# Performance work log

Hardware: AMD Instinct MI355X
Metric: run time of the kernel (lower is better)

The kernel has to match this reference:

```python
import jax, jax.numpy as jnp
import numpy as np

IN_CH_IMG = 256
CHANNELS = 256
NUM_CLASSES = 1
NUM_LAYERS = 4  # NUM_FC=3 -> 4 layers
IN_CH = IN_CH_IMG + 256  # pos-enc adds 256 channels
N_INST = 128
N_PTS = 2048

W_SIZES = [IN_CH * CHANNELS, CHANNELS * CHANNELS, CHANNELS * CHANNELS, CHANNELS * NUM_CLASSES]
B_SIZES = [CHANNELS, CHANNELS, CHANNELS, NUM_CLASSES]
NUM_PARAMS = sum(W_SIZES) + sum(B_SIZES)  # 263169


def setup_inputs() -> dict:
    key = jax.random.key(0)
    k1, k2, k3, k4 = jax.random.split(key, 4)
    return {
        "fine_grained_features": jax.random.normal(k1, (N_INST, IN_CH_IMG, N_PTS), dtype=jnp.float32),
        "point_coords": jax.random.uniform(k2, (N_INST, N_PTS, 2), dtype=jnp.float32),
        "parameters": jax.random.normal(k3, (N_INST, NUM_PARAMS), dtype=jnp.float32) * 0.05,
        "pe_gaussian": jax.random.normal(k4, (2, 128), dtype=jnp.float32),
    }


def _parse_params(params):
    # params: [N, NUM_PARAMS]. Weight blocks first, then bias blocks.
    n = params.shape[0]
    out_dims = [CHANNELS, CHANNELS, CHANNELS, NUM_CLASSES]
    in_dims = [IN_CH, CHANNELS, CHANNELS, CHANNELS]
    weights, biases = [], []
    off = 0
    for l in range(NUM_LAYERS):
        weights.append(params[:, off:off + W_SIZES[l]].reshape(n, out_dims[l], in_dims[l]))
        off += W_SIZES[l]
    for l in range(NUM_LAYERS):
        biases.append(params[:, off:off + B_SIZES[l]].reshape(n, out_dims[l], 1))
        off += B_SIZES[l]
    return weights, biases


def reference(fine_grained_features, point_coords, parameters, pe_gaussian):
    n, _, p = fine_grained_features.shape
    # Positional encoding: [N*P, 2] -> [N*P, 128] -> sin/cos -> [N, 256, P]
    loc = (2.0 * point_coords.reshape(n * p, 2) - 1.0) @ pe_gaussian
    loc = 2.0 * np.pi * loc
    pe = jnp.concatenate([jnp.sin(loc), jnp.cos(loc)], axis=1)  # [N*P, 256]
    pe = pe.reshape(n, p, 256).transpose(0, 2, 1)  # [N, 256, P]
    x = jnp.concatenate([pe, fine_grained_features], axis=1)  # [N, IN_CH, P]

    weights, biases = _parse_params(parameters)
    for i, (w, b) in enumerate(zip(weights, biases)):
        x = jnp.einsum('nck,ndc->ndk', x, w) + b
        if i < NUM_LAYERS - 1:
            x = jax.nn.relu(x)
    return x.reshape(-1, NUM_CLASSES, p)  # [N, 1, P]
```

## Files before the change

### kernel.cpp

```cpp
#include <hip/hip_runtime.h>
#include <hip/hip_fp16.h>


#define NI      128
#define NPTS    2048
#define CH      256
#define NPARAM  263169
#define PT      64
#define NTILES  (NPTS / PT)
#define ROWS    536

#define WOFF0   0
#define WOFF1   131072
#define WOFF2   196608
#define WOFF3   262144
#define BOFF0   262400
#define BOFF1   262656
#define BOFF2   262912
#define BOFF3   263168

#define PI_L0   0
#define PI_L1   131072
#define PI_L2   196608
#define PI_L3   262144
#define WS_PER_INST 262400
#define WS_BYTES ((size_t)NI * WS_PER_INST * 2)

typedef __fp16   h16x2 __attribute__((ext_vector_type(2)));
typedef _Float16 f16x8 __attribute__((ext_vector_type(8)));
typedef float    f32x4 __attribute__((ext_vector_type(4)));

union pack8 { h16x2 h[4]; f16x8 v; };

__global__ __launch_bounds__(256) void iph_prep(
    const float* __restrict__ params, _Float16* __restrict__ wsw)
{
    const int inst = blockIdx.y;
    const int r = blockIdx.x * 256 + threadIdx.x;
    if (r >= 32800) return;
    const float* __restrict__ P = params + (size_t)inst * NPARAM;
    _Float16* __restrict__ W = wsw + (size_t)inst * WS_PER_INST;

    int rl, woff, K, dst;
    if (r < 16384)      { rl = r;         woff = WOFF0; K = 512; dst = PI_L0; }
    else if (r < 24576) { rl = r - 16384; woff = WOFF1; K = 256; dst = PI_L1; }
    else if (r < 32768) { rl = r - 24576; woff = WOFF2; K = 256; dst = PI_L2; }
    else {
        const int e = (r - 32768) * 8;
        f16x8 v;
        #pragma unroll
        for (int j = 0; j < 8; ++j) v[j] = (_Float16)P[WOFF3 + e + j];
        *(f16x8*)&W[PI_L3 + e] = v;
        return;
    }
    const int e    = rl * 8;
    const int lane = rl & 63;
    const int cb   = (rl >> 6) & 15;
    const int ks   = rl >> 10;
    const int co   = (cb >> 1) * 32 + 2 * (lane & 15) + (cb & 1);
    const int k    = ks * 32 + (lane >> 4) * 8;
    const float* __restrict__ src = P + woff + co * K + k;
    f16x8 v;
    #pragma unroll
    for (int j = 0; j < 8; ++j) v[j] = (_Float16)src[j];
    *(f16x8*)&W[dst + e] = v;
}

__device__ __forceinline__ void issue_b2(const _Float16* p, f16x8& r0, f16x8& r1) {
    const unsigned long long a = (unsigned long long)p;
    asm volatile("global_load_dwordx4 %0, %2, off\n\t"
                 "global_load_dwordx4 %1, %2, off offset:1024"
                 : "=&v"(r0), "=&v"(r1)
                 : "v"(a));
}

template<int N>
__device__ __forceinline__ void wait_vm() {
    if constexpr (N >= 8)      asm volatile("s_waitcnt vmcnt(8)" ::: "memory");
    else if constexpr (N == 6) asm volatile("s_waitcnt vmcnt(6)" ::: "memory");
    else if constexpr (N == 4) asm volatile("s_waitcnt vmcnt(4)" ::: "memory");
    else if constexpr (N == 2) asm volatile("s_waitcnt vmcnt(2)" ::: "memory");
    else                       asm volatile("s_waitcnt vmcnt(0)" ::: "memory");
    __builtin_amdgcn_sched_barrier(0);
}

__device__ __forceinline__ void lgkm0_barrier() {
    asm volatile("s_waitcnt lgkmcnt(0)" ::: "memory");
    __builtin_amdgcn_s_barrier();
}

__device__ __forceinline__ void issue_pro(const _Float16* bp, f16x8 (&b0s)[5], f16x8 (&b1s)[5]) {
    #pragma unroll
    for (int i = 0; i < 4; ++i)
        issue_b2(bp + i * 8192, b0s[i], b1s[i]);
}

template<int NKS>
__device__ __forceinline__ void gemm_pipe(
    f32x4 (&acc)[4][2], const _Float16* bp, const _Float16* ap,
    f16x8 (&b0s)[5], f16x8 (&b1s)[5])
{
    #pragma unroll
    for (int ks = 0; ks < NKS; ++ks) {
        f16x8 a0 = *(const f16x8*)(ap + ks * 32);
        f16x8 a1 = *(const f16x8*)(ap + 16 * ROWS + ks * 32);
        f16x8 a2 = *(const f16x8*)(ap + 32 * ROWS + ks * 32);
        f16x8 a3 = *(const f16x8*)(ap + 48 * ROWS + ks * 32);
        if (ks + 4 < NKS)
            issue_b2(bp + (ks + 4) * 8192, b0s[(ks + 4) % 5], b1s[(ks + 4) % 5]);
        const int rem = NKS - 1 - ks;
        if (rem >= 4)      wait_vm<8>();
        else if (rem == 3) wait_vm<6>();
        else if (rem == 2) wait_vm<4>();
        else if (rem == 1) wait_vm<2>();
        else               wait_vm<0>();
        __builtin_amdgcn_s_setprio(1);
        acc[0][0] = __builtin_amdgcn_mfma_f32_16x16x32_f16(a0, b0s[ks % 5], acc[0][0], 0, 0, 0);
        acc[0][1] = __builtin_amdgcn_mfma_f32_16x16x32_f16(a0, b1s[ks % 5], acc[0][1], 0, 0, 0);
        acc[1][0] = __builtin_amdgcn_mfma_f32_16x16x32_f16(a1, b0s[ks % 5], acc[1][0], 0, 0, 0);
        acc[1][1] = __builtin_amdgcn_mfma_f32_16x16x32_f16(a1, b1s[ks % 5], acc[1][1], 0, 0, 0);
        acc[2][0] = __builtin_amdgcn_mfma_f32_16x16x32_f16(a2, b0s[ks % 5], acc[2][0], 0, 0, 0);
        acc[2][1] = __builtin_amdgcn_mfma_f32_16x16x32_f16(a2, b1s[ks % 5], acc[2][1], 0, 0, 0);
        acc[3][0] = __builtin_amdgcn_mfma_f32_16x16x32_f16(a3, b0s[ks % 5], acc[3][0], 0, 0, 0);
        acc[3][1] = __builtin_amdgcn_mfma_f32_16x16x32_f16(a3, b1s[ks % 5], acc[3][1], 0, 0, 0);
        __builtin_amdgcn_s_setprio(0);
    }
}

template<bool PREPPED>
__global__ __launch_bounds__(512, 4) void iph_main(
    const float* __restrict__ feat,
    const float* __restrict__ coords,
    const float* __restrict__ params,
    const _Float16* __restrict__ wsw,
    const float* __restrict__ peg,
    float* __restrict__ out)
{
    __shared__ _Float16 X[PT * ROWS];
    __shared__ float    partial[8][PT];

    const int bid  = blockIdx.x;
    const int inst = (bid & 7) | ((bid >> 8) << 3);
    const int tile = (bid >> 3) & 31;
    const int p0   = tile * PT;
    const int tid  = threadIdx.x;
    const int lane = tid & 63;
    const int wave = tid >> 6;
    const int l15  = lane & 15;
    const int hi   = lane >> 4;
    const float* __restrict__ P = params + (size_t)inst * NPARAM;
    const _Float16* __restrict__ WI = wsw + (size_t)inst * WS_PER_INST;

    const _Float16* bp0 = WI + PI_L0 + ((wave * 2) * 64 + lane) * 8;
    const _Float16* bp1 = WI + PI_L1 + ((wave * 2) * 64 + lane) * 8;
    const _Float16* bp2 = WI + PI_L2 + ((wave * 2) * 64 + lane) * 8;
    const _Float16* ap  = &X[l15 * ROWS + hi * 8];

    f16x8 s0[5], s1[5], t0[5], t1[5], u0[5], u1[5];

    if (PREPPED) issue_pro(bp0, s0, s1);

    {
        const int pt   = tid >> 3;
        const int part = tid & 7;
        const float2 cc = *(const float2*)&coords[((size_t)inst * NPTS + p0 + pt) * 2];
        const float a = 2.f * cc.x - 1.f;
        const float b = 2.f * cc.y - 1.f;
        float sv[16], cv[16];
        #pragma unroll
        for (int j = 0; j < 16; ++j) {
            const int f = part * 16 + j;
            float locr = a * peg[f] + b * peg[128 + f];
            locr -= floorf(locr);
            sv[j] = __builtin_amdgcn_sinf(locr);
            cv[j] = __builtin_amdgcn_cosf(locr);
        }
        pack8 q0, q1, c0, c1;
        #pragma unroll
        for (int q = 0; q < 4; ++q) {
            q0.h[q] = __builtin_amdgcn_cvt_pkrtz(sv[2*q],     sv[2*q + 1]);
            q1.h[q] = __builtin_amdgcn_cvt_pkrtz(sv[8 + 2*q], sv[9 + 2*q]);
            c0.h[q] = __builtin_amdgcn_cvt_pkrtz(cv[2*q],     cv[2*q + 1]);
            c1.h[q] = __builtin_amdgcn_cvt_pkrtz(cv[8 + 2*q], cv[9 + 2*q]);
        }
        _Float16* base = &X[pt * ROWS + part * 16];
        *(f16x8*)(base)           = q0.v;
        *(f16x8*)(base + 8)       = q1.v;
        *(f16x8*)(base + 128)     = c0.v;
        *(f16x8*)(base + 136)     = c1.v;
    }
    {
        const float* fbase = feat + (size_t)inst * CH * NPTS + p0 + lane;
        #pragma unroll
        for (int s = 0; s < 4; ++s) {
            const int c0i = s * 64 + wave * 8;
            float w8[8];
            #pragma unroll
            for (int j = 0; j < 8; ++j)
                w8[j] = fbase[(size_t)(c0i + j) * NPTS];
            pack8 pk;
            #pragma unroll
            for (int q = 0; q < 4; ++q)
                pk.h[q] = __builtin_amdgcn_cvt_pkrtz(w8[2*q], w8[2*q + 1]);
            *(f16x8*)&X[lane * ROWS + 256 + c0i] = pk.v;
        }
    }
    lgkm0_barrier();

    auto write_epilogue = [&](f32x4 (&acc)[4][2], const float2 bb) {
        #pragma unroll
        for (int mt = 0; mt < 4; ++mt) {
            #pragma unroll
            for (int r = 0; r < 4; ++r) {
                const float v0 = fmaxf(acc[mt][0][r] + bb.x, 0.f);
                const float v1 = fmaxf(acc[mt][1][r] + bb.y, 0.f);
                const h16x2 e = __builtin_amdgcn_cvt_pkrtz(v0, v1);
                const int pt = mt * 16 + hi * 4 + r;
                *(h16x2*)&X[pt * ROWS + wave * 32 + 2 * l15] = e;
            }
        }
    };

    auto gemm_simple = [&](f32x4 (&acc)[4][2], const float* pw, const int K) {
        for (int ks = 0; ks < (K >> 5); ++ks) {
            f16x8 bfrag[2];
            #pragma unroll
            for (int nt = 0; nt < 2; ++nt) {
                const int co = wave * 32 + 2 * l15 + nt;
                const float* wp = pw + (size_t)co * K + ks * 32 + hi * 8;
                float w8[8];
                __builtin_memcpy(w8, wp, 32);
                f16x8 bb;
                #pragma unroll
                for (int j = 0; j < 8; ++j) bb[j] = (_Float16)w8[j];
                bfrag[nt] = bb;
            }
            f16x8 afrag[4];
            #pragma unroll
            for (int mt = 0; mt < 4; ++mt)
                afrag[mt] = *(const f16x8*)&X[(mt * 16 + l15) * ROWS + ks * 32 + hi * 8];
            #pragma unroll
            for (int mt = 0; mt < 4; ++mt)
                #pragma unroll
                for (int nt = 0; nt < 2; ++nt)
                    acc[mt][nt] = __builtin_amdgcn_mfma_f32_16x16x32_f16(
                        afrag[mt], bfrag[nt], acc[mt][nt], 0, 0, 0);
        }
    };

    {
        f32x4 acc[4][2];
        #pragma unroll
        for (int mt = 0; mt < 4; ++mt)
            #pragma unroll
            for (int nt = 0; nt < 2; ++nt)
                acc[mt][nt] = (f32x4){0.f, 0.f, 0.f, 0.f};
        const float2 bb = *(const float2*)&P[BOFF0 + wave * 32 + 2 * l15];
        if (PREPPED) gemm_pipe<16>(acc, bp0, ap, s0, s1);
        else         gemm_simple(acc, P + WOFF0, 512);
        if (PREPPED) issue_pro(bp1, t0, t1);
        __builtin_amdgcn_s_barrier();
        write_epilogue(acc, bb);
        lgkm0_barrier();
    }
    {
        f32x4 acc[4][2];
        #pragma unroll
        for (int mt = 0; mt < 4; ++mt)
            #pragma unroll
            for (int nt = 0; nt < 2; ++nt)
                acc[mt][nt] = (f32x4){0.f, 0.f, 0.f, 0.f};
        const float2 bb = *(const float2*)&P[BOFF1 + wave * 32 + 2 * l15];
        if (PREPPED) gemm_pipe<8>(acc, bp1, ap, t0, t1);
        else         gemm_simple(acc, P + WOFF1, 256);
        if (PREPPED) issue_pro(bp2, u0, u1);
        __builtin_amdgcn_s_barrier();
        write_epilogue(acc, bb);
        lgkm0_barrier();
    }
    {
        f32x4 acc[4][2];
        #pragma unroll
        for (int mt = 0; mt < 4; ++mt)
            #pragma unroll
            for (int nt = 0; nt < 2; ++nt)
                acc[mt][nt] = (f32x4){0.f, 0.f, 0.f, 0.f};
        const float2 bb = *(const float2*)&P[BOFF2 + wave * 32 + 2 * l15];
        const float2 w3 = *(const float2*)&P[WOFF3 + wave * 32 + 2 * l15];
        if (PREPPED) gemm_pipe<8>(acc, bp2, ap, u0, u1);
        else         gemm_simple(acc, P + WOFF2, 256);
        #pragma unroll
        for (int mt = 0; mt < 4; ++mt) {
            #pragma unroll
            for (int r = 0; r < 4; ++r) {
                const float v0 = fmaxf(acc[mt][0][r] + bb.x, 0.f);
                const float v1 = fmaxf(acc[mt][1][r] + bb.y, 0.f);
                float s = v0 * w3.x + v1 * w3.y;
                s += __shfl_xor(s, 1);
                s += __shfl_xor(s, 2);
                s += __shfl_xor(s, 4);
                s += __shfl_xor(s, 8);
                if (l15 == 0)
                    partial[wave][mt * 16 + hi * 4 + r] = s;
            }
        }
        lgkm0_barrier();
        if (tid < PT) {
            float s = P[BOFF3];
            #pragma unroll
            for (int w = 0; w < 8; ++w) s += partial[w][tid];
            out[(size_t)inst * NPTS + p0 + tid] = s;
        }
    }
}

extern "C" void kernel_launch(void* const* d_in, const int* in_sizes, int n_in,
                              void* d_out, int out_size, void* d_ws, size_t ws_size,
                              hipStream_t stream) {
    (void)in_sizes; (void)n_in; (void)out_size;
    const float* feat   = (const float*)d_in[0];
    const float* coords = (const float*)d_in[1];
    const float* params = (const float*)d_in[2];
    const float* peg    = (const float*)d_in[3];
    float* out = (float*)d_out;

    dim3 grid(NI * NTILES);
    dim3 block(512);

    if (ws_size >= WS_BYTES) {
        _Float16* wsw = (_Float16*)d_ws;
        iph_prep<<<dim3(129, 128), dim3(256), 0, stream>>>(params, wsw);
        iph_main<true><<<grid, block, 0, stream>>>(feat, coords, params, wsw, peg, out);
    } else {
        iph_main<false><<<grid, block, 0, stream>>>(feat, coords, params,
                                                    (const _Float16*)d_ws, peg, out);
    }
}
```

Before: 214.9 us.

## Switch GEMM layers to 32x32x16 MFMA with 8-deep single-load weight pipeline

Replaces the 16x16x32 MFMA tiling (4x2 accumulator tiles per wave) with two 32x32x16 MFMAs per k-step. The prepacked weight layout, LDS A-fragment addressing, epilogue and final reduction are reworked to match. The weight prefetch becomes one dwordx4 load per k-step with an 8-deep ring instead of paired loads 4 deep, and bias loads are hoisted to the kernel start. The aim is fewer MFMA issues and LDS A-reads per FLOP. In exchange the epilogue now writes scalar fp16 values to LDS instead of packed pairs, and k-steps are smaller.

After: 264.6 us. 1.23x slower.

```diff
diff --git a/kernel.cpp b/kernel.cpp
--- a/kernel.cpp
+++ b/kernel.cpp
@@ -26,9 +26,9 @@
 #define WS_PER_INST 262400
 #define WS_BYTES ((size_t)NI * WS_PER_INST * 2)
 
-typedef __fp16   h16x2 __attribute__((ext_vector_type(2)));
-typedef _Float16 f16x8 __attribute__((ext_vector_type(8)));
-typedef float    f32x4 __attribute__((ext_vector_type(4)));
+typedef __fp16   h16x2  __attribute__((ext_vector_type(2)));
+typedef _Float16 f16x8  __attribute__((ext_vector_type(8)));
+typedef float    f32x16 __attribute__((ext_vector_type(16)));
 
 union pack8 { h16x2 h[4]; f16x8 v; };
 
@@ -55,10 +55,10 @@
     }
     const int e    = rl * 8;
     const int lane = rl & 63;
-    const int cb   = (rl >> 6) & 15;
-    const int ks   = rl >> 10;
-    const int co   = (cb >> 1) * 32 + 2 * (lane & 15) + (cb & 1);
-    const int k    = ks * 32 + (lane >> 4) * 8;
+    const int cb   = (rl >> 6) & 7;
+    const int ks   = rl >> 9;
+    const int co   = cb * 32 + (lane & 31);
+    const int k    = ks * 16 + (lane >> 5) * 8;
     const float* __restrict__ src = P + woff + co * K + k;
     f16x8 v;
     #pragma unroll
@@ -66,20 +66,20 @@
     *(f16x8*)&W[dst + e] = v;
 }
 
-__device__ __forceinline__ void issue_b2(const _Float16* p, f16x8& r0, f16x8& r1) {
+__device__ __forceinline__ void issue_b1(const _Float16* p, f16x8& r0) {
     const unsigned long long a = (unsigned long long)p;
-    asm volatile("global_load_dwordx4 %0, %2, off\n\t"
-                 "global_load_dwordx4 %1, %2, off offset:1024"
-                 : "=&v"(r0), "=&v"(r1)
-                 : "v"(a));
+    asm volatile("global_load_dwordx4 %0, %1, off" : "=&v"(r0) : "v"(a));
 }
 
 template<int N>
 __device__ __forceinline__ void wait_vm() {
-    if constexpr (N >= 8)      asm volatile("s_waitcnt vmcnt(8)" ::: "memory");
+    if constexpr (N >= 7)      asm volatile("s_waitcnt vmcnt(7)" ::: "memory");
     else if constexpr (N == 6) asm volatile("s_waitcnt vmcnt(6)" ::: "memory");
+    else if constexpr (N == 5) asm volatile("s_waitcnt vmcnt(5)" ::: "memory");
     else if constexpr (N == 4) asm volatile("s_waitcnt vmcnt(4)" ::: "memory");
+    else if constexpr (N == 3) asm volatile("s_waitcnt vmcnt(3)" ::: "memory");
     else if constexpr (N == 2) asm volatile("s_waitcnt vmcnt(2)" ::: "memory");
+    else if constexpr (N == 1) asm volatile("s_waitcnt vmcnt(1)" ::: "memory");
     else                       asm volatile("s_waitcnt vmcnt(0)" ::: "memory");
     __builtin_amdgcn_sched_barrier(0);
 }
@@ -89,41 +89,35 @@
     __builtin_amdgcn_s_barrier();
 }
 
-__device__ __forceinline__ void issue_pro(const _Float16* bp, f16x8 (&b0s)[5], f16x8 (&b1s)[5]) {
+__device__ __forceinline__ void issue_pro8(const _Float16* bp, f16x8 (&q)[8]) {
     #pragma unroll
-    for (int i = 0; i < 4; ++i)
-        issue_b2(bp + i * 8192, b0s[i], b1s[i]);
+    for (int i = 0; i < 8; ++i) issue_b1(bp + i * 4096, q[i]);
 }
 
 template<int NKS>
 __device__ __forceinline__ void gemm_pipe(
-    f32x4 (&acc)[4][2], const _Float16* bp, const _Float16* ap,
-    f16x8 (&b0s)[5], f16x8 (&b1s)[5])
+    f32x16& acc0, f32x16& acc1, const _Float16* bp, const _Float16* ap,
+    f16x8 (&q)[8])
 {
     #pragma unroll
     for (int ks = 0; ks < NKS; ++ks) {
-        f16x8 a0 = *(const f16x8*)(ap + ks * 32);
-        f16x8 a1 = *(const f16x8*)(ap + 16 * ROWS + ks * 32);
-        f16x8 a2 = *(const f16x8*)(ap + 32 * ROWS + ks * 32);
-        f16x8 a3 = *(const f16x8*)(ap + 48 * ROWS + ks * 32);
-        if (ks + 4 < NKS)
-            issue_b2(bp + (ks + 4) * 8192, b0s[(ks + 4) % 5], b1s[(ks + 4) % 5]);
+        f16x8 a0 = *(const f16x8*)(ap + ks * 16);
+        f16x8 a1 = *(const f16x8*)(ap + 32 * ROWS + ks * 16);
         const int rem = NKS - 1 - ks;
-        if (rem >= 4)      wait_vm<8>();
-        else if (rem == 3) wait_vm<6>();
-        else if (rem == 2) wait_vm<4>();
-        else if (rem == 1) wait_vm<2>();
+        if (rem >= 7)      wait_vm<7>();
+        else if (rem == 6) wait_vm<6>();
+        else if (rem == 5) wait_vm<5>();
+        else if (rem == 4) wait_vm<4>();
+        else if (rem == 3) wait_vm<3>();
+        else if (rem == 2) wait_vm<2>();
+        else if (rem == 1) wait_vm<1>();
         else               wait_vm<0>();
         __builtin_amdgcn_s_setprio(1);
-        acc[0][0] = __builtin_amdgcn_mfma_f32_16x16x32_f16(a0, b0s[ks % 5], acc[0][0], 0, 0, 0);
-        acc[0][1] = __builtin_amdgcn_mfma_f32_16x16x32_f16(a0, b1s[ks % 5], acc[0][1], 0, 0, 0);
-        acc[1][0] = __builtin_amdgcn_mfma_f32_16x16x32_f16(a1, b0s[ks % 5], acc[1][0], 0, 0, 0);
-        acc[1][1] = __builtin_amdgcn_mfma_f32_16x16x32_f16(a1, b1s[ks % 5], acc[1][1], 0, 0, 0);
-        acc[2][0] = __builtin_amdgcn_mfma_f32_16x16x32_f16(a2, b0s[ks % 5], acc[2][0], 0, 0, 0);
-        acc[2][1] = __builtin_amdgcn_mfma_f32_16x16x32_f16(a2, b1s[ks % 5], acc[2][1], 0, 0, 0);
-        acc[3][0] = __builtin_amdgcn_mfma_f32_16x16x32_f16(a3, b0s[ks % 5], acc[3][0], 0, 0, 0);
-        acc[3][1] = __builtin_amdgcn_mfma_f32_16x16x32_f16(a3, b1s[ks % 5], acc[3][1], 0, 0, 0);
+        acc0 = __builtin_amdgcn_mfma_f32_32x32x16_f16(a0, q[ks & 7], acc0, 0, 0, 0);
+        acc1 = __builtin_amdgcn_mfma_f32_32x32x16_f16(a1, q[ks & 7], acc1, 0, 0, 0);
         __builtin_amdgcn_s_setprio(0);
+        if (ks + 8 < NKS)
+            issue_b1(bp + (ks + 8) * 4096, q[ks & 7]);
     }
 }
 
@@ -146,19 +140,24 @@
     const int tid  = threadIdx.x;
     const int lane = tid & 63;
     const int wave = tid >> 6;
-    const int l15  = lane & 15;
-    const int hi   = lane >> 4;
+    const int l31  = lane & 31;
+    const int sel  = lane >> 5;
     const float* __restrict__ P = params + (size_t)inst * NPARAM;
     const _Float16* __restrict__ WI = wsw + (size_t)inst * WS_PER_INST;
 
-    const _Float16* bp0 = WI + PI_L0 + ((wave * 2) * 64 + lane) * 8;
-    const _Float16* bp1 = WI + PI_L1 + ((wave * 2) * 64 + lane) * 8;
-    const _Float16* bp2 = WI + PI_L2 + ((wave * 2) * 64 + lane) * 8;
-    const _Float16* ap  = &X[l15 * ROWS + hi * 8];
-
-    f16x8 s0[5], s1[5], t0[5], t1[5], u0[5], u1[5];
-
-    if (PREPPED) issue_pro(bp0, s0, s1);
+    const _Float16* bp0 = WI + PI_L0 + (wave * 64 + lane) * 8;
+    const _Float16* bp1 = WI + PI_L1 + (wave * 64 + lane) * 8;
+    const _Float16* bp2 = WI + PI_L2 + (wave * 64 + lane) * 8;
+    const _Float16* ap  = &X[l31 * ROWS + sel * 8];
+
+    const float bb0 = P[BOFF0 + wave * 32 + l31];
+    const float bb1 = P[BOFF1 + wave * 32 + l31];
+    const float bb2 = P[BOFF2 + wave * 32 + l31];
+    const float w3  = P[WOFF3 + wave * 32 + l31];
+
+    f16x8 qa[8], qb[8], qc[8];
+
+    if (PREPPED) issue_pro8(bp0, qa);
 
     {
         const int pt   = tid >> 3;
@@ -207,101 +206,69 @@
     }
     lgkm0_barrier();
 
-    auto write_epilogue = [&](f32x4 (&acc)[4][2], const float2 bb) {
-        #pragma unroll
-        for (int mt = 0; mt < 4; ++mt) {
-            #pragma unroll
-            for (int r = 0; r < 4; ++r) {
-                const float v0 = fmaxf(acc[mt][0][r] + bb.x, 0.f);
-                const float v1 = fmaxf(acc[mt][1][r] + bb.y, 0.f);
-                const h16x2 e = __builtin_amdgcn_cvt_pkrtz(v0, v1);
-                const int pt = mt * 16 + hi * 4 + r;
-                *(h16x2*)&X[pt * ROWS + wave * 32 + 2 * l15] = e;
+    auto write_epilogue = [&](const f32x16& a0, const f32x16& a1, const float bb) {
+        #pragma unroll
+        for (int r = 0; r < 16; ++r) {
+            const int ptrow = (r & 3) + 8 * (r >> 2) + 4 * sel;
+            const float v0 = fmaxf(a0[r] + bb, 0.f);
+            const float v1 = fmaxf(a1[r] + bb, 0.f);
+            X[ptrow * ROWS + wave * 32 + l31]        = (_Float16)v0;
+            X[(32 + ptrow) * ROWS + wave * 32 + l31] = (_Float16)v1;
+        }
+    };
+
+    auto gemm_simple = [&](f32x16& a0c, f32x16& a1c, const float* pw, const int K) {
+        for (int ks = 0; ks < (K >> 4); ++ks) {
+            const float* wp = pw + (size_t)(wave * 32 + l31) * K + ks * 16 + sel * 8;
+            float w8[8];
+            __builtin_memcpy(w8, wp, 32);
+            f16x8 bf;
+            #pragma unroll
+            for (int j = 0; j < 8; ++j) bf[j] = (_Float16)w8[j];
+            f16x8 a0 = *(const f16x8*)(ap + ks * 16);
+            f16x8 a1 = *(const f16x8*)(ap + 32 * ROWS + ks * 16);
+            a0c = __builtin_amdgcn_mfma_f32_32x32x16_f16(a0, bf, a0c, 0, 0, 0);
+            a1c = __builtin_amdgcn_mfma_f32_32x32x16_f16(a1, bf, a1c, 0, 0, 0);
+        }
+    };
+
+    const f32x16 zero = {0.f,0.f,0.f,0.f,0.f,0.f,0.f,0.f,0.f,0.f,0.f,0.f,0.f,0.f,0.f,0.f};
+
+    {
+        f32x16 acc0 = zero, acc1 = zero;
+        if (PREPPED) gemm_pipe<32>(acc0, acc1, bp0, ap, qa);
+        else         gemm_simple(acc0, acc1, P + WOFF0, 512);
+        if (PREPPED) issue_pro8(bp1, qb);
+        __builtin_amdgcn_s_barrier();
+        write_epilogue(acc0, acc1, bb0);
+        lgkm0_barrier();
+    }
+    {
+        f32x16 acc0 = zero, acc1 = zero;
+        if (PREPPED) gemm_pipe<16>(acc0, acc1, bp1, ap, qb);
+        else         gemm_simple(acc0, acc1, P + WOFF1, 256);
+        if (PREPPED) issue_pro8(bp2, qc);
+        __builtin_amdgcn_s_barrier();
+        write_epilogue(acc0, acc1, bb1);
+        lgkm0_barrier();
+    }
+    {
+        f32x16 acc0 = zero, acc1 = zero;
+        if (PREPPED) gemm_pipe<16>(acc0, acc1, bp2, ap, qc);
+        else         gemm_simple(acc0, acc1, P + WOFF2, 256);
+        #pragma unroll
+        for (int r = 0; r < 16; ++r) {
+            const int ptrow = (r & 3) + 8 * (r >> 2) + 4 * sel;
+            float s0 = fmaxf(acc0[r] + bb2, 0.f) * w3;
+            float s1 = fmaxf(acc1[r] + bb2, 0.f) * w3;
+            #pragma unroll
+            for (int d = 1; d <= 16; d <<= 1) {
+                s0 += __shfl_xor(s0, d);
+                s1 += __shfl_xor(s1, d);
             }
-        }
-    };
-
-    auto gemm_simple = [&](f32x4 (&acc)[4][2], const float* pw, const int K) {
-        for (int ks = 0; ks < (K >> 5); ++ks) {
-            f16x8 bfrag[2];
-            #pragma unroll
-            for (int nt = 0; nt < 2; ++nt) {
-                const int co = wave * 32 + 2 * l15 + nt;
-                const float* wp = pw + (size_t)co * K + ks * 32 + hi * 8;
-                float w8[8];
-                __builtin_memcpy(w8, wp, 32);
-                f16x8 bb;
-                #pragma unroll
-                for (int j = 0; j < 8; ++j) bb[j] = (_Float16)w8[j];
-                bfrag[nt] = bb;
-            }
-            f16x8 afrag[4];
-            #pragma unroll
-            for (int mt = 0; mt < 4; ++mt)
-                afrag[mt] = *(const f16x8*)&X[(mt * 16 + l15) * ROWS + ks * 32 + hi * 8];
-            #pragma unroll
-            for (int mt = 0; mt < 4; ++mt)
-                #pragma unroll
-                for (int nt = 0; nt < 2; ++nt)
-                    acc[mt][nt] = __builtin_amdgcn_mfma_f32_16x16x32_f16(
-                        afrag[mt], bfrag[nt], acc[mt][nt], 0, 0, 0);
-        }
-    };
-
-    {
-        f32x4 acc[4][2];
-        #pragma unroll
-        for (int mt = 0; mt < 4; ++mt)
-            #pragma unroll
-            for (int nt = 0; nt < 2; ++nt)
-                acc[mt][nt] = (f32x4){0.f, 0.f, 0.f, 0.f};
-        const float2 bb = *(const float2*)&P[BOFF0 + wave * 32 + 2 * l15];
-        if (PREPPED) gemm_pipe<16>(acc, bp0, ap, s0, s1);
-        else         gemm_simple(acc, P + WOFF0, 512);
-        if (PREPPED) issue_pro(bp1, t0, t1);
-        __builtin_amdgcn_s_barrier();
-        write_epilogue(acc, bb);
-        lgkm0_barrier();
-    }
-    {
-        f32x4 acc[4][2];
-        #pragma unroll
-        for (int mt = 0; mt < 4; ++mt)
-            #pragma unroll
-            for (int nt = 0; nt < 2; ++nt)
-                acc[mt][nt] = (f32x4){0.f, 0.f, 0.f, 0.f};
-        const float2 bb = *(const float2*)&P[BOFF1 + wave * 32 + 2 * l15];
-        if (PREPPED) gemm_pipe<8>(acc, bp1, ap, t0, t1);
-        else         gemm_simple(acc, P + WOFF1, 256);
-        if (PREPPED) issue_pro(bp2, u0, u1);
-        __builtin_amdgcn_s_barrier();
-        write_epilogue(acc, bb);
-        lgkm0_barrier();
-    }
-    {
-        f32x4 acc[4][2];
-        #pragma unroll
-        for (int mt = 0; mt < 4; ++mt)
-            #pragma unroll
-            for (int nt = 0; nt < 2; ++nt)
-                acc[mt][nt] = (f32x4){0.f, 0.f, 0.f, 0.f};
-        const float2 bb = *(const float2*)&P[BOFF2 + wave * 32 + 2 * l15];
-        const float2 w3 = *(const float2*)&P[WOFF3 + wave * 32 + 2 * l15];
-        if (PREPPED) gemm_pipe<8>(acc, bp2, ap, u0, u1);
-        else         gemm_simple(acc, P + WOFF2, 256);
-        #pragma unroll
-        for (int mt = 0; mt < 4; ++mt) {
-            #pragma unroll
-            for (int r = 0; r < 4; ++r) {
-                const float v0 = fmaxf(acc[mt][0][r] + bb.x, 0.f);
-                const float v1 = fmaxf(acc[mt][1][r] + bb.y, 0.f);
-                float s = v0 * w3.x + v1 * w3.y;
-                s += __shfl_xor(s, 1);
-                s += __shfl_xor(s, 2);
-                s += __shfl_xor(s, 4);
-                s += __shfl_xor(s, 8);
-                if (l15 == 0)
-                    partial[wave][mt * 16 + hi * 4 + r] = s;
+            if (l31 == 0) {
+                partial[wave][ptrow]      = s0;
+                partial[wave][32 + ptrow] = s1;
             }
         }
         lgkm0_barrier();
```

## Double point tile to 128 so each block reuses weights over more points

Applied to the files above, without the earlier changes.

Raises the point tile per block from 64 to 128. Each wave now holds 8 M-tiles of accumulators and runs 8 A-fragment loads per k-step, and the positional-encoding and feature staging loops are remapped to the larger tile. The aim is to halve how often each instance's per-layer weights are streamed from global memory, doubling MFMA work per weight fetch. Bias and final-layer weight loads are also hoisted to kernel entry. In exchange, LDS use roughly doubles to about 137KB, allowing only one block per CU, and register pressure rises, with the occupancy hint dropped from launch bounds.

Measured after the change: 246.7 us. +14.8%, slower.

```diff
diff --git a/kernel.cpp b/kernel.cpp
--- a/kernel.cpp
+++ b/kernel.cpp
@@ -6,7 +6,7 @@
 #define NPTS    2048
 #define CH      256
 #define NPARAM  263169
-#define PT      64
+#define PT      128
 #define NTILES  (NPTS / PT)
 #define ROWS    536
 
@@ -97,15 +97,15 @@
 
 template<int NKS>
 __device__ __forceinline__ void gemm_pipe(
-    f32x4 (&acc)[4][2], const _Float16* bp, const _Float16* ap,
+    f32x4 (&acc)[8][2], const _Float16* bp, const _Float16* ap,
     f16x8 (&b0s)[5], f16x8 (&b1s)[5])
 {
     #pragma unroll
     for (int ks = 0; ks < NKS; ++ks) {
-        f16x8 a0 = *(const f16x8*)(ap + ks * 32);
-        f16x8 a1 = *(const f16x8*)(ap + 16 * ROWS + ks * 32);
-        f16x8 a2 = *(const f16x8*)(ap + 32 * ROWS + ks * 32);
-        f16x8 a3 = *(const f16x8*)(ap + 48 * ROWS + ks * 32);
+        f16x8 a[8];
+        #pragma unroll
+        for (int mt = 0; mt < 8; ++mt)
+            a[mt] = *(const f16x8*)(ap + mt * 16 * ROWS + ks * 32);
         if (ks + 4 < NKS)
             issue_b2(bp + (ks + 4) * 8192, b0s[(ks + 4) % 5], b1s[(ks + 4) % 5]);
         const int rem = NKS - 1 - ks;
@@ -115,20 +115,17 @@
         else if (rem == 1) wait_vm<2>();
         else               wait_vm<0>();
         __builtin_amdgcn_s_setprio(1);
-        acc[0][0] = __builtin_amdgcn_mfma_f32_16x16x32_f16(a0, b0s[ks % 5], acc[0][0], 0, 0, 0);
-        acc[0][1] = __builtin_amdgcn_mfma_f32_16x16x32_f16(a0, b1s[ks % 5], acc[0][1], 0, 0, 0);
-        acc[1][0] = __builtin_amdgcn_mfma_f32_16x16x32_f16(a1, b0s[ks % 5], acc[1][0], 0, 0, 0);
-        acc[1][1] = __builtin_amdgcn_mfma_f32_16x16x32_f16(a1, b1s[ks % 5], acc[1][1], 0, 0, 0);
-        acc[2][0] = __builtin_amdgcn_mfma_f32_16x16x32_f16(a2, b0s[ks % 5], acc[2][0], 0, 0, 0);
-        acc[2][1] = __builtin_amdgcn_mfma_f32_16x16x32_f16(a2, b1s[ks % 5], acc[2][1], 0, 0, 0);
-        acc[3][0] = __builtin_amdgcn_mfma_f32_16x16x32_f16(a3, b0s[ks % 5], acc[3][0], 0, 0, 0);
-        acc[3][1] = __builtin_amdgcn_mfma_f32_16x16x32_f16(a3, b1s[ks % 5], acc[3][1], 0, 0, 0);
+        #pragma unroll
+        for (int mt = 0; mt < 8; ++mt) {
+            acc[mt][0] = __builtin_amdgcn_mfma_f32_16x16x32_f16(a[mt], b0s[ks % 5], acc[mt][0], 0, 0, 0);
+            acc[mt][1] = __builtin_amdgcn_mfma_f32_16x16x32_f16(a[mt], b1s[ks % 5], acc[mt][1], 0, 0, 0);
+        }
         __builtin_amdgcn_s_setprio(0);
     }
 }
 
 template<bool PREPPED>
-__global__ __launch_bounds__(512, 4) void iph_main(
+__global__ __launch_bounds__(512) void iph_main(
     const float* __restrict__ feat,
     const float* __restrict__ coords,
     const float* __restrict__ params,
@@ -140,8 +137,8 @@
     __shared__ float    partial[8][PT];
 
     const int bid  = blockIdx.x;
-    const int inst = (bid & 7) | ((bid >> 8) << 3);
-    const int tile = (bid >> 3) & 31;
+    const int inst = (bid & 7) | ((bid >> 7) << 3);
+    const int tile = (bid >> 3) & 15;
     const int p0   = tile * PT;
     const int tid  = threadIdx.x;
     const int lane = tid & 63;
@@ -156,60 +153,65 @@
     const _Float16* bp2 = WI + PI_L2 + ((wave * 2) * 64 + lane) * 8;
     const _Float16* ap  = &X[l15 * ROWS + hi * 8];
 
+    const float2 bb0 = *(const float2*)&P[BOFF0 + wave * 32 + 2 * l15];
+    const float2 bb1 = *(const float2*)&P[BOFF1 + wave * 32 + 2 * l15];
+    const float2 bb2 = *(const float2*)&P[BOFF2 + wave * 32 + 2 * l15];
+    const float2 w3  = *(const float2*)&P[WOFF3 + wave * 32 + 2 * l15];
+
     f16x8 s0[5], s1[5], t0[5], t1[5], u0[5], u1[5];
 
     if (PREPPED) issue_pro(bp0, s0, s1);
 
     {
-        const int pt   = tid >> 3;
-        const int part = tid & 7;
+        const int pt   = tid >> 2;
+        const int part = tid & 3;
         const float2 cc = *(const float2*)&coords[((size_t)inst * NPTS + p0 + pt) * 2];
         const float a = 2.f * cc.x - 1.f;
         const float b = 2.f * cc.y - 1.f;
-        float sv[16], cv[16];
-        #pragma unroll
-        for (int j = 0; j < 16; ++j) {
-            const int f = part * 16 + j;
+        float sv[32], cv[32];
+        #pragma unroll
+        for (int j = 0; j < 32; ++j) {
+            const int f = part * 32 + j;
             float locr = a * peg[f] + b * peg[128 + f];
             locr -= floorf(locr);
             sv[j] = __builtin_amdgcn_sinf(locr);
             cv[j] = __builtin_amdgcn_cosf(locr);
         }
-        pack8 q0, q1, c0, c1;
-        #pragma unroll
-        for (int q = 0; q < 4; ++q) {
-            q0.h[q] = __builtin_amdgcn_cvt_pkrtz(sv[2*q],     sv[2*q + 1]);
-            q1.h[q] = __builtin_amdgcn_cvt_pkrtz(sv[8 + 2*q], sv[9 + 2*q]);
-            c0.h[q] = __builtin_amdgcn_cvt_pkrtz(cv[2*q],     cv[2*q + 1]);
-            c1.h[q] = __builtin_amdgcn_cvt_pkrtz(cv[8 + 2*q], cv[9 + 2*q]);
-        }
-        _Float16* base = &X[pt * ROWS + part * 16];
-        *(f16x8*)(base)           = q0.v;
-        *(f16x8*)(base + 8)       = q1.v;
-        *(f16x8*)(base + 128)     = c0.v;
-        *(f16x8*)(base + 136)     = c1.v;
-    }
-    {
-        const float* fbase = feat + (size_t)inst * CH * NPTS + p0 + lane;
-        #pragma unroll
-        for (int s = 0; s < 4; ++s) {
-            const int c0i = s * 64 + wave * 8;
+        _Float16* base = &X[pt * ROWS + part * 32];
+        #pragma unroll
+        for (int c = 0; c < 4; ++c) {
+            pack8 ps, pc;
+            #pragma unroll
+            for (int q = 0; q < 4; ++q) {
+                ps.h[q] = __builtin_amdgcn_cvt_pkrtz(sv[c*8 + 2*q], sv[c*8 + 2*q + 1]);
+                pc.h[q] = __builtin_amdgcn_cvt_pkrtz(cv[c*8 + 2*q], cv[c*8 + 2*q + 1]);
+            }
+            *(f16x8*)(base + c * 8)       = ps.v;
+            *(f16x8*)(base + 128 + c * 8) = pc.v;
+        }
+    }
+    {
+        const int p  = tid & 127;
+        const int cg = tid >> 7;
+        const float* fbase = feat + (size_t)inst * CH * NPTS + (size_t)(cg * 64) * NPTS + p0 + p;
+        #pragma unroll
+        for (int s = 0; s < 8; ++s) {
             float w8[8];
             #pragma unroll
             for (int j = 0; j < 8; ++j)
-                w8[j] = fbase[(size_t)(c0i + j) * NPTS];
+                w8[j] = fbase[(size_t)(s * 8 + j) * NPTS];
             pack8 pk;
             #pragma unroll
             for (int q = 0; q < 4; ++q)
                 pk.h[q] = __builtin_amdgcn_cvt_pkrtz(w8[2*q], w8[2*q + 1]);
-            *(f16x8*)&X[lane * ROWS + 256 + c0i] = pk.v;
+            *(f16x8*)&X[p * ROWS + 256 + cg * 64 + s * 8] = pk.v;
         }
     }
     lgkm0_barrier();
 
-    auto write_epilogue = [&](f32x4 (&acc)[4][2], const float2 bb) {
-        #pragma unroll
-        for (int mt = 0; mt < 4; ++mt) {
+    auto write_epilogue = [&](f32x4 (&acc)[8][2], const float2 bb) {
+        #pragma unroll
+        for (int mt = 0; mt < 8; ++mt) {
             #pragma unroll
             for (int r = 0; r < 4; ++r) {
                 const float v0 = fmaxf(acc[mt][0][r] + bb.x, 0.f);
@@ -221,7 +223,7 @@
         }
     };
 
-    auto gemm_simple = [&](f32x4 (&acc)[4][2], const float* pw, const int K) {
+    auto gemm_simple = [&](f32x4 (&acc)[8][2], const float* pw, const int K) {
         for (int ks = 0; ks < (K >> 5); ++ks) {
             f16x8 bfrag[2];
             #pragma unroll
@@ -235,66 +237,58 @@
                 for (int j = 0; j < 8; ++j) bb[j] = (_Float16)w8[j];
                 bfrag[nt] = bb;
             }
-            f16x8 afrag[4];
-            #pragma unroll
-            for (int mt = 0; mt < 4; ++mt)
-                afrag[mt] = *(const f16x8*)&X[(mt * 16 + l15) * ROWS + ks * 32 + hi * 8];
-            #pragma unroll
-            for (int mt = 0; mt < 4; ++mt)
-                #pragma unroll
-                for (int nt = 0; nt < 2; ++nt)
-                    acc[mt][nt] = __builtin_amdgcn_mfma_f32_16x16x32_f16(
-                        afrag[mt], bfrag[nt], acc[mt][nt], 0, 0, 0);
+            #pragma unroll
+            for (int mt = 0; mt < 8; ++mt) {
+                f16x8 af = *(const f16x8*)&X[(mt * 16 + l15) * ROWS + ks * 32 + hi * 8];
+                acc[mt][0] = __builtin_amdgcn_mfma_f32_16x16x32_f16(af, bfrag[0], acc[mt][0], 0, 0, 0);
+                acc[mt][1] = __builtin_amdgcn_mfma_f32_16x16x32_f16(af, bfrag[1], acc[mt][1], 0, 0, 0);
+            }
         }
     };
 
     {
-        f32x4 acc[4][2];
-        #pragma unroll
-        for (int mt = 0; mt < 4; ++mt)
+        f32x4 acc[8][2];
+        #pragma unroll
+        for (int mt = 0; mt < 8; ++mt)
             #pragma unroll
             for (int nt = 0; nt < 2; ++nt)
                 acc[mt][nt] = (f32x4){0.f, 0.f, 0.f, 0.f};
-        const float2 bb = *(const float2*)&P[BOFF0 + wave * 32 + 2 * l15];
         if (PREPPED) gemm_pipe<16>(acc, bp0, ap, s0, s1);
         else         gemm_simple(acc, P + WOFF0, 512);
         if (PREPPED) issue_pro(bp1, t0, t1);
         __builtin_amdgcn_s_barrier();
-        write_epilogue(acc, bb);
+        write_epilogue(acc, bb0);
         lgkm0_barrier();
     }
     {
-        f32x4 acc[4][2];
-        #pragma unroll
-        for (int mt = 0; mt < 4; ++mt)
+        f32x4 acc[8][2];
+        #pragma unroll
+        for (int mt = 0; mt < 8; ++mt)
             #pragma unroll
             for (int nt = 0; nt < 2; ++nt)
                 acc[mt][nt] = (f32x4){0.f, 0.f, 0.f, 0.f};
-        const float2 bb = *(const float2*)&P[BOFF1 + wave * 32 + 2 * l15];
         if (PREPPED) gemm_pipe<8>(acc, bp1, ap, t0, t1);
         else         gemm_simple(acc, P + WOFF1, 256);
         if (PREPPED) issue_pro(bp2, u0, u1);
         __builtin_amdgcn_s_barrier();
-        write_epilogue(acc, bb);
+        write_epilogue(acc, bb1);
         lgkm0_barrier();
     }
     {
-        f32x4 acc[4][2];
-        #pragma unroll
-        for (int mt = 0; mt < 4; ++mt)
+        f32x4 acc[8][2];
+        #pragma unroll
+        for (int mt = 0; mt < 8; ++mt)
             #pragma unroll
             for (int nt = 0; nt < 2; ++nt)
                 acc[mt][nt] = (f32x4){0.f, 0.f, 0.f, 0.f};
-        const float2 bb = *(const float2*)&P[BOFF2 + wave * 32 + 2 * l15];
-        const float2 w3 = *(const float2*)&P[WOFF3 + wave * 32 + 2 * l15];
         if (PREPPED) gemm_pipe<8>(acc, bp2, ap, u0, u1);
         else         gemm_simple(acc, P + WOFF2, 256);
         #pragma unroll
-        for (int mt = 0; mt < 4; ++mt) {
+        for (int mt = 0; mt < 8; ++mt) {
             #pragma unroll
             for (int r = 0; r < 4; ++r) {
-                const float v0 = fmaxf(acc[mt][0][r] + bb.x, 0.f);
-                const float v1 = fmaxf(acc[mt][1][r] + bb.y, 0.f);
+                const float v0 = fmaxf(acc[mt][0][r] + bb2.x, 0.f);
+                const float v1 = fmaxf(acc[mt][1][r] + bb2.y, 0.f);
                 float s = v0 * w3.x + v1 * w3.y;
                 s += __shfl_xor(s, 1);
                 s += __shfl_xor(s, 2);
```
